# Performance work log

Measured on AMD Instinct MI355X. Metric: run time of the kernel, lower is better.

Reference implementation:

```python
import jax, jax.numpy as jnp
import numpy as np

DEPTH, DIM, HEADS, MLP_HID, POS_DIM, PROJ_DIM, NCLS, INP = 5, 128, 8, 256, 128, 128, 1000, 35
EPS = 1e-5

def _ln(x, g, b):
    m = x.mean(-1, keepdims=True)
    v = ((x - m) ** 2).mean(-1, keepdims=True)
    return (x - m) / jnp.sqrt(v + EPS) * g + b

def _gelu(x):
    return jax.nn.gelu(x, approximate=False)  # torch nn.GELU default (erf)

def setup_inputs() -> dict:
    key = jax.random.key(0)
    ks = iter(jax.random.split(key, 80))
    nxt = lambda: next(ks)
    B, N = 8, 1024
    w = lambda *s: (jax.random.normal(nxt(), s, jnp.float32) / np.sqrt(s[-2]).astype(np.float32))
    z = lambda *s: jnp.zeros(s, jnp.float32)
    o = lambda *s: jnp.ones(s, jnp.float32)
    node_feat = jax.random.normal(nxt(), (B, N, 3), jnp.float32)
    a = (jax.random.uniform(nxt(), (B, N, N)) < 0.01).astype(jnp.float32)
    adj = jnp.maximum(a, a.transpose(0, 2, 1))  # symmetric 0/1 adjacency
    lapl = jax.random.normal(nxt(), (B, N, 32), jnp.float32) * 0.1
    d = dict(
        node_feat=node_feat, adj=adj, lapl=lapl,
        cls_token=jax.random.normal(nxt(), (1, 1, DIM), jnp.float32),
        pe_w1=w(INP, 2 * INP), pe_b1=z(2 * INP),
        pe_w2=w(2 * INP, 2 * INP), pe_b2=z(2 * INP),
        pe_w3=w(2 * INP, 2 * INP), pe_b3=z(2 * INP),
        pe_lng=o(2 * INP), pe_lnb=z(2 * INP),
        pe_w4=w(2 * INP, POS_DIM), pe_b4=z(POS_DIM),
        blk_ln1_g=o(DEPTH, DIM), blk_ln1_b=z(DEPTH, DIM),
        blk_qkv_w=w(DEPTH, DIM, 3 * HEADS * DIM),
        blk_proj_w=w(DEPTH, HEADS * DIM, DIM), blk_proj_b=z(DEPTH, DIM),
        blk_gamma_w=jax.random.uniform(nxt(), (DEPTH, DIM, 2), jnp.float32) * 0.01,
        blk_gamma_b=z(DEPTH, 2),
        blk_ln2_g=o(DEPTH, DIM), blk_ln2_b=z(DEPTH, DIM),
        blk_mlp_w1=w(DEPTH, DIM, MLP_HID), blk_mlp_b1=z(DEPTH, MLP_HID),
        blk_mlp_w2=w(DEPTH, MLP_HID, DIM), blk_mlp_b2=z(DEPTH, DIM),
        head_lng=o(DIM), head_lnb=z(DIM), head_w=w(DIM, DIM), head_b=z(DIM),
        proj_w1=w(DIM, PROJ_DIM), proj_b1=z(PROJ_DIM),
        proj_w2=w(PROJ_DIM, PROJ_DIM), proj_b2=z(PROJ_DIM),
        proj_w3=w(PROJ_DIM, PROJ_DIM), proj_b3=z(PROJ_DIM),
        proj_lng=o(PROJ_DIM), proj_lnb=z(PROJ_DIM),
        proj_w4=w(PROJ_DIM, NCLS), proj_b4=z(NCLS),
    )
    return d

def reference(node_feat, adj, lapl, cls_token, pe_w1, pe_b1, pe_w2, pe_b2, pe_w3, pe_b3,
              pe_lng, pe_lnb, pe_w4, pe_b4, blk_ln1_g, blk_ln1_b, blk_qkv_w, blk_proj_w,
              blk_proj_b, blk_gamma_w, blk_gamma_b, blk_ln2_g, blk_ln2_b, blk_mlp_w1,
              blk_mlp_b1, blk_mlp_w2, blk_mlp_b2, head_lng, head_lnb, head_w, head_b,
              proj_w1, proj_b1, proj_w2, proj_b2, proj_w3, proj_b3, proj_lng, proj_lnb,
              proj_w4, proj_b4):
    B, N, _ = node_feat.shape
    M = N + 1
    # positional-encoding MLP on concatenated [node_feat | lapl] (inp_dim = 35)
    x = jnp.concatenate([node_feat, lapl], axis=2)
    x = _gelu(x @ pe_w1 + pe_b1)
    x = _gelu(x @ pe_w2 + pe_b2)
    x = _gelu(x @ pe_w3 + pe_b3)
    x = _ln(x, pe_lng, pe_lnb) @ pe_w4 + pe_b4  # [B,N,DIM]
    x = jnp.concatenate([jnp.broadcast_to(cls_token, (B, 1, DIM)), x], axis=1)  # [B,M,DIM]
    # adjacency with cls row/col, adj_cls[:,0,0] = 1
    adj_cls = jnp.zeros((B, M, M), x.dtype).at[:, 0, 0].set(1.0).at[:, 1:, 1:].set(adj)
    scale = DIM ** (-0.5)
    for i in range(DEPTH):
        h = _ln(x, blk_ln1_g[i], blk_ln1_b[i])
        qkv = (h @ blk_qkv_w[i]).reshape(B, M, 3, HEADS, DIM).transpose(2, 0, 3, 1, 4)
        q, k, v = qkv[0], qkv[1], qkv[2]  # each [B,H,M,D]
        attn = jnp.einsum('bhnd,bhmd->bhnm', q, k) * scale
        gamma = jnp.exp(h @ blk_gamma_w[i] + blk_gamma_b[i])  # [B,M,2], use_exp=True
        attn = gamma[:, None, :, 0:1] * attn + gamma[:, None, :, 1:2] * adj_cls[:, None]
        attn = jax.nn.softmax(attn, axis=-1)
        o = jnp.einsum('bhnm,bhmd->bhnd', attn, v).transpose(0, 2, 1, 3).reshape(B, M, HEADS * DIM)
        x = o @ blk_proj_w[i] + blk_proj_b[i] + h  # residual from normed input (as in source)
        h2 = _ln(x, blk_ln2_g[i], blk_ln2_b[i])
        x = _gelu(h2 @ blk_mlp_w1[i] + blk_mlp_b1[i]) @ blk_mlp_w2[i] + blk_mlp_b2[i] + h2
    c = x[:, 0]
    c = _ln(c, head_lng, head_lnb) @ head_w + head_b  # mlp_head
    p = _gelu(c @ proj_w1 + proj_b1)
    p = _gelu(p @ proj_w2 + proj_b2)
    p = _gelu(p @ proj_w3 + proj_b3)
    p = _ln(p, proj_lng, proj_lnb) @ proj_w4 + proj_b4
    return (c, p)
```

## Files before the change

kernel.cpp:

```cpp
#include <hip/hip_runtime.h>
#include <hip/hip_bf16.h>
#include <math.h>

#define NB 8
#define NSEQ 1024
#define M_ 1025
#define ROWS (NB * M_)
#define DIMC 128
#define NHEADS 8
#define QKV3 3072
#define PEROWS (NB * NSEQ)
#define ACS 1088

typedef __attribute__((ext_vector_type(8))) short bf16x8;
typedef __attribute__((ext_vector_type(4))) float f32x4;

__device__ __forceinline__ float gelu_f(float x) {
  return 0.5f * x * (1.f + erff(x * 0.70710678118654752440f));
}

__device__ __forceinline__ unsigned short f2bf(float f) {
  __hip_bfloat16 h = __float2bfloat16(f);
  return *reinterpret_cast<unsigned short*>(&h);
}

__device__ __forceinline__ float bf2f(unsigned short u) {
  union { unsigned int i; float f; } c;
  c.i = ((unsigned int)u) << 16;
  return c.f;
}

__device__ __forceinline__ void g2lds16(const void* g, void* l) {
  __builtin_amdgcn_global_load_lds(
      (__attribute__((address_space(1))) void*)(g),
      (__attribute__((address_space(3))) void*)(l), 16, 0, 0);
}

template<int K, int KP, int C, int SS, int DOGELU>
__device__ __forceinline__ void pe_stage(
    int tid, const float* __restrict__ W, const float* __restrict__ B,
    const float* src, float* dst, float (*wb)[128])
{
  for (int i = tid; i < K * C; i += 128) wb[i / C][i % C] = W[i];
  if (tid < C) {
#pragma unroll
    for (int k = K; k < KP; ++k) wb[k][tid] = 0.f;
  }
  __syncthreads();
  if (tid < C) {
    float acc[16];
#pragma unroll
    for (int r = 0; r < 16; ++r) acc[r] = B[tid];
#pragma unroll 1
    for (int k4 = 0; k4 < KP; k4 += 4) {
      const float w0 = wb[k4 + 0][tid];
      const float w1 = wb[k4 + 1][tid];
      const float w2 = wb[k4 + 2][tid];
      const float w3 = wb[k4 + 3][tid];
#pragma unroll
      for (int r = 0; r < 16; ++r) {
        const float4 av = *(const float4*)&src[r * SS + k4];
        acc[r] = fmaf(av.x, w0, acc[r]);
        acc[r] = fmaf(av.y, w1, acc[r]);
        acc[r] = fmaf(av.z, w2, acc[r]);
        acc[r] = fmaf(av.w, w3, acc[r]);
      }
    }
#pragma unroll
    for (int r = 0; r < 16; ++r) dst[r * 72 + tid] = DOGELU ? gelu_f(acc[r]) : acc[r];
  }
  __syncthreads();
}

__global__ __launch_bounds__(128) void pe_fused_k(
    const float* __restrict__ nf, const float* __restrict__ lp,
    const float* __restrict__ w1, const float* __restrict__ b1,
    const float* __restrict__ w2, const float* __restrict__ b2,
    const float* __restrict__ w3, const float* __restrict__ b3,
    const float* __restrict__ lng, const float* __restrict__ lnb,
    const float* __restrict__ w4, const float* __restrict__ b4,
    float* __restrict__ x)
{
  __shared__ float sIn[16][36];
  __shared__ float sX[16][72];
  __shared__ float sY[16][72];
  __shared__ float wb[72][128];
  const int tid = threadIdx.x;
  const int r0 = blockIdx.x * 16;

  for (int i = tid; i < 16 * 35; i += 128) {
    const int r = i / 35, c = i - r * 35;
    const int gr = r0 + r;
    sIn[r][c] = (c < 3) ? nf[(size_t)gr * 3 + c] : lp[(size_t)gr * 32 + (c - 3)];
  }
  if (tid < 16) {
    sIn[tid][35] = 0.f;
    sX[tid][70] = 0.f; sX[tid][71] = 0.f;
    sY[tid][70] = 0.f; sY[tid][71] = 0.f;
  }
  __syncthreads();

  pe_stage<35, 36, 70, 36, 1>(tid, w1, b1, &sIn[0][0], &sX[0][0], wb);
  pe_stage<70, 72, 70, 72, 1>(tid, w2, b2, &sX[0][0], &sY[0][0], wb);
  pe_stage<70, 72, 70, 72, 1>(tid, w3, b3, &sY[0][0], &sX[0][0], wb);

  if (tid < 16) {
    float m = 0.f;
    for (int d = 0; d < 70; ++d) m += sX[tid][d];
    m *= (1.f / 70.f);
    float v = 0.f;
    for (int d = 0; d < 70; ++d) { const float t = sX[tid][d] - m; v += t * t; }
    const float inv = rsqrtf(v * (1.f / 70.f) + 1e-5f);
    for (int d = 0; d < 70; ++d) sX[tid][d] = (sX[tid][d] - m) * inv * lng[d] + lnb[d];
  }
  __syncthreads();

  {
    for (int i = tid; i < 70 * 128; i += 128) wb[i >> 7][i & 127] = w4[i];
#pragma unroll
    for (int k = 70; k < 72; ++k) wb[k][tid] = 0.f;
    __syncthreads();
    float acc[16];
#pragma unroll
    for (int r = 0; r < 16; ++r) acc[r] = b4[tid];
#pragma unroll 1
    for (int k4 = 0; k4 < 72; k4 += 4) {
      const float w0 = wb[k4 + 0][tid];
      const float w1v = wb[k4 + 1][tid];
      const float w2v = wb[k4 + 2][tid];
      const float w3v = wb[k4 + 3][tid];
#pragma unroll
      for (int r = 0; r < 16; ++r) {
        const float4 av = *(const float4*)&sX[r][k4];
        acc[r] = fmaf(av.x, w0, acc[r]);
        acc[r] = fmaf(av.y, w1v, acc[r]);
        acc[r] = fmaf(av.z, w2v, acc[r]);
        acc[r] = fmaf(av.w, w3v, acc[r]);
      }
    }
#pragma unroll
    for (int r = 0; r < 16; ++r) {
      const int gr = r0 + r;
      x[(size_t)(gr + gr / 1024 + 1) * DIMC + tid] = acc[r];
    }
  }
}

template<int ACT, int OBF, int RES>
__global__ __launch_bounds__(256) void mgemm_k(
    const unsigned short* __restrict__ Xb, const unsigned short* __restrict__ Wt,
    const float* __restrict__ bias, const float* __restrict__ res,
    void* __restrict__ outp, int rows, int K, int N)
{
  __shared__ unsigned short sX[64][72];
  __shared__ unsigned short sW[64][72];
  const int tid = threadIdx.x;
  const int w = tid >> 6, lane = tid & 63;
  const int col = lane & 15, quad = lane >> 4;
  const int r0 = blockIdx.x * 64, n0 = blockIdx.y * 64;
  const int lr = tid >> 2, lc = tid & 3;
  const int xrow = min(r0 + lr, rows - 1);
  const unsigned short* xsrc = Xb + (size_t)xrow * K + lc * 8;
  const unsigned short* wsrc = Wt + (size_t)(n0 + lr) * K + lc * 8;

  f32x4 acc[4];
#pragma unroll
  for (int t = 0; t < 4; ++t) acc[t] = (f32x4){0.f, 0.f, 0.f, 0.f};

  for (int k0 = 0; k0 < K; k0 += 64) {
    __syncthreads();
    *(uint4*)&sX[lr][lc * 8]      = *(const uint4*)(xsrc + k0);
    *(uint4*)&sX[lr][lc * 8 + 32] = *(const uint4*)(xsrc + k0 + 32);
    *(uint4*)&sW[lr][lc * 8]      = *(const uint4*)(wsrc + k0);
    *(uint4*)&sW[lr][lc * 8 + 32] = *(const uint4*)(wsrc + k0 + 32);
    __syncthreads();
    const bf16x8 aX0 = *(const bf16x8*)&sX[w * 16 + col][quad * 8];
    const bf16x8 aX1 = *(const bf16x8*)&sX[w * 16 + col][32 + quad * 8];
#pragma unroll
    for (int t = 0; t < 4; ++t) {
      const bf16x8 bW0 = *(const bf16x8*)&sW[t * 16 + col][quad * 8];
      const bf16x8 bW1 = *(const bf16x8*)&sW[t * 16 + col][32 + quad * 8];
      acc[t] = __builtin_amdgcn_mfma_f32_16x16x32_bf16(aX0, bW0, acc[t], 0, 0, 0);
      acc[t] = __builtin_amdgcn_mfma_f32_16x16x32_bf16(aX1, bW1, acc[t], 0, 0, 0);
    }
  }
  const int gr_base = r0 + w * 16 + quad * 4;
#pragma unroll
  for (int t = 0; t < 4; ++t) {
    const int n = n0 + t * 16 + col;
    const float bv = bias ? bias[n] : 0.f;
#pragma unroll
    for (int r = 0; r < 4; ++r) {
      const int gr = gr_base + r;
      if (gr < rows) {
        float v = acc[t][r] + bv;
        if (ACT) v = gelu_f(v);
        if (RES) v += res[(size_t)gr * N + n];
        if (OBF) ((unsigned short*)outp)[(size_t)gr * N + n] = f2bf(v);
        else     ((float*)outp)[(size_t)gr * N + n] = v;
      }
    }
  }
}

template<int DOLN, int GAMMA, int WRITEX>
__global__ __launch_bounds__(256) void mgemm_ln_k(
    const unsigned short* __restrict__ Xb, const unsigned short* __restrict__ Wt,
    const float* __restrict__ bias, const float* __restrict__ res,
    const float* __restrict__ lng, const float* __restrict__ lnb,
    const float* __restrict__ gw, const float* __restrict__ gb,
    float* __restrict__ xout, float* __restrict__ h,
    unsigned short* __restrict__ hb, float* __restrict__ gamout,
    int rows, int K)
{
  __shared__ unsigned short sX[32][72];
  __shared__ unsigned short sW[128][72];
  __shared__ float redS[2][32];
  __shared__ float redQ[2][32];
  __shared__ float redA0[2][32];
  __shared__ float redA1[2][32];
  const int tid = threadIdx.x;
  const int w = tid >> 6, lane = tid & 63;
  const int col = lane & 15, quad = lane >> 4;
  const int rg = w >> 1, ch = w & 1;
  const int r0 = blockIdx.x * 32;

  f32x4 acc[4];
#pragma unroll
  for (int t = 0; t < 4; ++t) acc[t] = (f32x4){0.f, 0.f, 0.f, 0.f};

  for (int k0 = 0; k0 < K; k0 += 64) {
    __syncthreads();
    {
      const int row = tid >> 3, c = tid & 7;
      const int xrow = min(r0 + row, rows - 1);
      *(uint4*)&sX[row][c * 8] = *(const uint4*)(Xb + (size_t)xrow * K + k0 + c * 8);
    }
#pragma unroll
    for (int l = 0; l < 4; ++l) {
      const int idx = l * 256 + tid;
      const int row = idx >> 3, c = idx & 7;
      *(uint4*)&sW[row][c * 8] = *(const uint4*)(Wt + (size_t)row * K + k0 + c * 8);
    }
    __syncthreads();
    const bf16x8 aX0 = *(const bf16x8*)&sX[rg * 16 + col][quad * 8];
    const bf16x8 aX1 = *(const bf16x8*)&sX[rg * 16 + col][32 + quad * 8];
#pragma unroll
    for (int t = 0; t < 4; ++t) {
      const bf16x8 bW0 = *(const bf16x8*)&sW[ch * 64 + t * 16 + col][quad * 8];
      const bf16x8 bW1 = *(const bf16x8*)&sW[ch * 64 + t * 16 + col][32 + quad * 8];
      acc[t] = __builtin_amdgcn_mfma_f32_16x16x32_bf16(aX0, bW0, acc[t], 0, 0, 0);
      acc[t] = __builtin_amdgcn_mfma_f32_16x16x32_bf16(aX1, bW1, acc[t], 0, 0, 0);
    }
  }

  const int gr_base = r0 + rg * 16 + quad * 4;
  float val[4][4];
#pragma unroll
  for (int r = 0; r < 4; ++r) {
    const int grc = min(gr_base + r, rows - 1);
#pragma unroll
    for (int t = 0; t < 4; ++t) {
      const int n = ch * 64 + t * 16 + col;
      val[t][r] = acc[t][r] + bias[n] + res[(size_t)grc * DIMC + n];
    }
  }
  if (WRITEX) {
#pragma unroll
    for (int r = 0; r < 4; ++r) {
      const int gr = gr_base + r;
      if (gr < rows) {
#pragma unroll
        for (int t = 0; t < 4; ++t)
          xout[(size_t)gr * DIMC + ch * 64 + t * 16 + col] = val[t][r];
      }
    }
  }
  if (DOLN) {
#pragma unroll
    for (int r = 0; r < 4; ++r) {
      float s = 0.f, q = 0.f;
#pragma unroll
      for (int t = 0; t < 4; ++t) { s += val[t][r]; q = fmaf(val[t][r], val[t][r], q); }
      s += __shfl_xor(s, 1); s += __shfl_xor(s, 2);
      s += __shfl_xor(s, 4); s += __shfl_xor(s, 8);
      q += __shfl_xor(q, 1); q += __shfl_xor(q, 2);
      q += __shfl_xor(q, 4); q += __shfl_xor(q, 8);
      if (col == 0) {
        const int rl = rg * 16 + quad * 4 + r;
        redS[ch][rl] = s;
        redQ[ch][rl] = q;
      }
    }
    __syncthreads();
    float lg[4], lb[4], gwa[4], gwb[4];
#pragma unroll
    for (int t = 0; t < 4; ++t) {
      const int n = ch * 64 + t * 16 + col;
      lg[t] = lng[n];
      lb[t] = lnb[n];
      if (GAMMA) { gwa[t] = gw[2 * n]; gwb[t] = gw[2 * n + 1]; }
    }
#pragma unroll
    for (int r = 0; r < 4; ++r) {
      const int rl = rg * 16 + quad * 4 + r;
      const int gr = gr_base + r;
      const float S = redS[0][rl] + redS[1][rl];
      const float Q = redQ[0][rl] + redQ[1][rl];
      const float mean = S * (1.f / 128.f);
      const float var = Q * (1.f / 128.f) - mean * mean;
      const float inv = rsqrtf(var + 1e-5f);
      float a0 = 0.f, a1 = 0.f;
#pragma unroll
      for (int t = 0; t < 4; ++t) {
        const float o = (val[t][r] - mean) * inv * lg[t] + lb[t];
        if (gr < rows) {
          const int n = ch * 64 + t * 16 + col;
          h[(size_t)gr * DIMC + n] = o;
          hb[(size_t)gr * DIMC + n] = f2bf(o);
        }
        if (GAMMA) { a0 = fmaf(o, gwa[t], a0); a1 = fmaf(o, gwb[t], a1); }
      }
      if (GAMMA) {
        a0 += __shfl_xor(a0, 1); a0 += __shfl_xor(a0, 2);
        a0 += __shfl_xor(a0, 4); a0 += __shfl_xor(a0, 8);
        a1 += __shfl_xor(a1, 1); a1 += __shfl_xor(a1, 2);
        a1 += __shfl_xor(a1, 4); a1 += __shfl_xor(a1, 8);
        if (col == 0) { redA0[ch][rl] = a0; redA1[ch][rl] = a1; }
      }
    }
    if (GAMMA) {
      __syncthreads();
#pragma unroll
      for (int r = 0; r < 4; ++r) {
        const int rl = rg * 16 + quad * 4 + r;
        const int gr = gr_base + r;
        if (ch == 0 && col == 0 && gr < rows) {
          gamout[(size_t)gr * 2 + 0] = expf(redA0[0][rl] + redA0[1][rl] + gb[0]);
          gamout[(size_t)gr * 2 + 1] = expf(redA1[0][rl] + redA1[1][rl] + gb[1]);
        }
      }
    }
  }
}

template<int OBF, int VT>
__global__ __launch_bounds__(256) void mgemm128_k(
    const unsigned short* __restrict__ Xb, const unsigned short* __restrict__ Wt,
    const float* __restrict__ bias, void* __restrict__ outp,
    unsigned short* __restrict__ vtp, int rows, int K, int N)
{
  __shared__ unsigned short sX[128][72];
  __shared__ unsigned short sW[128][72];
  const int tid = threadIdx.x;
  const int w = tid >> 6, lane = tid & 63;
  const int col = lane & 15, quad = lane >> 4;
  const int wr = w >> 1, wc = w & 1;
  const int r0 = blockIdx.x * 128, n0 = blockIdx.y * 128;

  f32x4 acc[4][4];
#pragma unroll
  for (int i = 0; i < 4; ++i)
#pragma unroll
    for (int j = 0; j < 4; ++j) acc[i][j] = (f32x4){0.f, 0.f, 0.f, 0.f};

  for (int k0 = 0; k0 < K; k0 += 64) {
    __syncthreads();
#pragma unroll
    for (int l = 0; l < 4; ++l) {
      const int idx = l * 256 + tid;
      const int row = idx >> 3, c = idx & 7;
      const int xrow = min(r0 + row, rows - 1);
      *(uint4*)&sX[row][c * 8] = *(const uint4*)(Xb + (size_t)xrow * K + k0 + c * 8);
      *(uint4*)&sW[row][c * 8] = *(const uint4*)(Wt + (size_t)(n0 + row) * K + k0 + c * 8);
    }
    __syncthreads();
    bf16x8 aX[4][2];
#pragma unroll
    for (int i = 0; i < 4; ++i) {
      aX[i][0] = *(const bf16x8*)&sX[wr * 64 + i * 16 + col][quad * 8];
      aX[i][1] = *(const bf16x8*)&sX[wr * 64 + i * 16 + col][32 + quad * 8];
    }
#pragma unroll
    for (int j = 0; j < 4; ++j) {
      const bf16x8 b0 = *(const bf16x8*)&sW[wc * 64 + j * 16 + col][quad * 8];
      const bf16x8 b1 = *(const bf16x8*)&sW[wc * 64 + j * 16 + col][32 + quad * 8];
#pragma unroll
      for (int i = 0; i < 4; ++i) {
        acc[i][j] = __builtin_amdgcn_mfma_f32_16x16x32_bf16(aX[i][0], b0, acc[i][j], 0, 0, 0);
        acc[i][j] = __builtin_amdgcn_mfma_f32_16x16x32_bf16(aX[i][1], b1, acc[i][j], 0, 0, 0);
      }
    }
  }
  const bool dovt = VT && (n0 >= 2048);
#pragma unroll
  for (int i = 0; i < 4; ++i) {
    const int gr_base = r0 + wr * 64 + i * 16 + quad * 4;
    int bb[4], mm[4];
    if (dovt) {
#pragma unroll
      for (int r = 0; r < 4; ++r) {
        const int gr = gr_base + r;
        bb[r] = gr / 1025;
        mm[r] = gr - bb[r] * 1025;
      }
    }
#pragma unroll
    for (int j = 0; j < 4; ++j) {
      const int n = n0 + wc * 64 + j * 16 + col;
      const float bv = bias ? bias[n] : 0.f;
      const int hh = (n - 2048) >> 7;
      const int d  = (n - 2048) & 127;
#pragma unroll
      for (int r = 0; r < 4; ++r) {
        const int gr = gr_base + r;
        if (gr < rows) {
          const float v = acc[i][j][r] + bv;
          const unsigned short bf = f2bf(v);
          if (OBF) ((unsigned short*)outp)[(size_t)gr * N + n] = bf;
          else     ((float*)outp)[(size_t)gr * N + n] = v;
          if (dovt) vtp[(((size_t)(bb[r] * NHEADS + hh) * DIMC + d) * ACS) + mm[r]] = bf;
        }
      }
    }
  }
}

__global__ __launch_bounds__(256) void ln_rows_k(
    const float* __restrict__ in, float* __restrict__ out,
    unsigned short* __restrict__ outb,
    const float* __restrict__ g, const float* __restrict__ b,
    const float* __restrict__ gw, const float* __restrict__ gb,
    float* __restrict__ gamout, int rows, int D)
{
  const int wv = (blockIdx.x * blockDim.x + threadIdx.x) >> 6;
  const int lane = threadIdx.x & 63;
  if (wv >= rows) return;
  const float* r = in + (size_t)wv * D;
  float s = 0.f;
  for (int d = lane; d < D; d += 64) s += r[d];
  for (int off = 32; off; off >>= 1) s += __shfl_down(s, off);
  const float mean = __shfl(s, 0) / (float)D;
  float v = 0.f;
  for (int d = lane; d < D; d += 64) { float t = r[d] - mean; v += t * t; }
  for (int off = 32; off; off >>= 1) v += __shfl_down(v, off);
  const float inv = rsqrtf(__shfl(v, 0) / (float)D + 1e-5f);
  float* orow = out + (size_t)wv * D;
  float a0 = 0.f, a1 = 0.f;
  for (int d = lane; d < D; d += 64) {
    const float o = (r[d] - mean) * inv * g[d] + b[d];
    orow[d] = o;
    if (outb) outb[(size_t)wv * D + d] = f2bf(o);
    if (gw) { a0 = fmaf(o, gw[2 * d], a0); a1 = fmaf(o, gw[2 * d + 1], a1); }
  }
  if (gw) {
    for (int off = 32; off; off >>= 1) { a0 += __shfl_down(a0, off); a1 += __shfl_down(a1, off); }
    if (lane == 0) {
      gamout[(size_t)wv * 2 + 0] = expf(a0 + gb[0]);
      gamout[(size_t)wv * 2 + 1] = expf(a1 + gb[1]);
    }
  }
}

__global__ __launch_bounds__(256) void adjp_k(const float* __restrict__ adj,
                                              unsigned long long* __restrict__ adjp)
{
  const int n = blockIdx.x;
  const int b = blockIdx.y;
  const int wv = threadIdx.x >> 6, lane = threadIdx.x & 63;
  for (int w = wv; w < 17; w += 4) {
    const int m = w * 64 + lane;
    float av = 0.f;
    if (n == 0) av = (m == 0) ? 1.f : 0.f;
    else if (m >= 1 && m <= NSEQ) av = adj[((size_t)b * NSEQ + (n - 1)) * NSEQ + (m - 1)];
    const unsigned long long mask = __ballot(av != 0.f);
    if (lane == 0) adjp[((size_t)b * M_ + n) * 17 + w] = mask;
  }
}

__global__ void wtrans_k(const float* __restrict__ W, unsigned short* __restrict__ Wt,
                         int K, int N)
{
  __shared__ float t[32][33];
  const int k0 = blockIdx.x * 32, n0 = blockIdx.y * 32;
  const float* Wd = W + (size_t)blockIdx.z * K * N;
  unsigned short* Wtd = Wt + (size_t)blockIdx.z * K * N;
  for (int i = threadIdx.y; i < 32; i += 8)
    t[i][threadIdx.x] = Wd[(size_t)(k0 + i) * N + n0 + threadIdx.x];
  __syncthreads();
  for (int i = threadIdx.y; i < 32; i += 8)
    Wtd[(size_t)(n0 + i) * K + k0 + threadIdx.x] = f2bf(t[threadIdx.x][i]);
}

__global__ __launch_bounds__(512) void attn_mfma_k(
    const unsigned short* __restrict__ qkv, const float* __restrict__ gamma,
    const unsigned long long* __restrict__ adjp, const unsigned short* __restrict__ vt,
    unsigned short* __restrict__ o)
{
  __shared__ unsigned short sK[2][64][128];
  __shared__ unsigned short sVt[2][128][64];
  __shared__ unsigned short sP[256][64];

  const int hh = blockIdx.x, qt = blockIdx.y, b = blockIdx.z;
  const int tid = threadIdx.x;
  const int w = tid >> 6;
  const int lane = tid & 63;
  const int col = lane & 15;
  const int quad = lane >> 4;
  const int qbase = qt * 256 + w * 32;
  const float scale = 0.088388347648318447f;

  bf16x8 aQ[2][4];
#pragma unroll
  for (int rg = 0; rg < 2; ++rg) {
    const int qrow = qbase + rg * 16 + col;
    const unsigned short* qp = qkv + ((size_t)(b * M_ + qrow)) * QKV3 + hh * DIMC + quad * 8;
#pragma unroll
    for (int c = 0; c < 4; ++c) aQ[rg][c] = *(const bf16x8*)(qp + c * 32);
  }
  float g0[2][4], g1[2][4];
  int adjo[2][4];
#pragma unroll
  for (int rg = 0; rg < 2; ++rg)
#pragma unroll
    for (int r = 0; r < 4; ++r) {
      const int nc = qbase + rg * 16 + quad * 4 + r;
      g0[rg][r] = gamma[(size_t)(b * M_ + nc) * 2 + 0] * scale;
      g1[rg][r] = gamma[(size_t)(b * M_ + nc) * 2 + 1];
      adjo[rg][r] = (b * M_ + nc) * 17;
    }

  float l_i[2][4] = {{0.f, 0.f, 0.f, 0.f}, {0.f, 0.f, 0.f, 0.f}};
  f32x4 Oacc[2][8];
#pragma unroll
  for (int rg = 0; rg < 2; ++rg)
#pragma unroll
    for (int t = 0; t < 8; ++t) Oacc[rg][t] = (f32x4){0.f, 0.f, 0.f, 0.f};

  const size_t vtbase = ((size_t)(b * NHEADS + hh)) * DIMC * ACS;

  auto stageK = [&](int buf, int kt_) {
#pragma unroll
    for (int l = 0; l < 2; ++l) {
      const int m = l * 32 + w * 4 + (lane >> 4);
      const int gm = min(kt_ * 64 + m, 1024);
      const unsigned short* src = qkv + ((size_t)(b * M_ + gm)) * QKV3 + 1024
                                  + hh * DIMC + (((lane & 15) ^ (m & 7)) * 8);
      g2lds16(src, &sK[buf][l * 32 + w * 4][0]);
    }
  };
  auto stageV = [&](int buf, int kt_) {
#pragma unroll
    for (int l = 0; l < 2; ++l) {
      const int d = l * 64 + w * 8 + (lane >> 3);
      const unsigned short* src = vt + vtbase + (size_t)d * ACS + kt_ * 64
                                  + (((lane & 7) ^ (d & 7)) * 8);
      g2lds16(src, &sVt[buf][l * 64 + w * 8][0]);
    }
  };

  stageK(0, 0);
  stageV(0, 0);

  int cur = 0;
  for (int kt = 0; kt < 17; ++kt) {
    const int m0 = kt * 64;
    asm volatile("s_waitcnt vmcnt(0)" ::: "memory");
    __builtin_amdgcn_s_barrier();
    __builtin_amdgcn_sched_barrier(0);

    const bool more = (kt < 16);
    if (more) {
      stageK(cur ^ 1, kt + 1);
      stageV(cur ^ 1, kt + 1);
    }

    unsigned long long mk[2][4];
#pragma unroll
    for (int rg = 0; rg < 2; ++rg)
#pragma unroll
      for (int r = 0; r < 4; ++r) mk[rg][r] = adjp[adjo[rg][r] + kt];

    f32x4 Sacc[2][4];
#pragma unroll
    for (int rg = 0; rg < 2; ++rg)
#pragma unroll
      for (int t = 0; t < 4; ++t) Sacc[rg][t] = (f32x4){0.f, 0.f, 0.f, 0.f};
    __builtin_amdgcn_s_setprio(1);
#pragma unroll
    for (int t = 0; t < 4; ++t) {
#pragma unroll
      for (int c = 0; c < 4; ++c) {
        const bf16x8 bK = *(const bf16x8*)&sK[cur][t * 16 + col][((c * 4 + quad) ^ (col & 7)) * 8];
        Sacc[0][t] = __builtin_amdgcn_mfma_f32_16x16x32_bf16(aQ[0][c], bK, Sacc[0][t], 0, 0, 0);
        Sacc[1][t] = __builtin_amdgcn_mfma_f32_16x16x32_bf16(aQ[1][c], bK, Sacc[1][t], 0, 0, 0);
      }
    }
    __builtin_amdgcn_s_setprio(0);

#pragma unroll
    for (int t = 0; t < 4; ++t) {
      const int m = m0 + t * 16 + col;
      const bool mv = (m < M_);
      const int chb = t * 2 + (col >> 3);
      const int sh = t * 16 + col;
#pragma unroll
      for (int rg = 0; rg < 2; ++rg)
#pragma unroll
        for (int r = 0; r < 4; ++r) {
          const float bias = ((mk[rg][r] >> sh) & 1ull) ? g1[rg][r] : 0.f;
          const float s = fmaf(g0[rg][r], Sacc[rg][t][r], bias);
          const float pv = mv ? __expf(s) : 0.f;
          l_i[rg][r] += pv;
          const int ql = w * 32 + rg * 16 + quad * 4 + r;
          sP[ql][((chb ^ (ql & 7)) * 8) + (col & 7)] = f2bf(pv);
        }
    }

    __builtin_amdgcn_s_setprio(1);
#pragma unroll
    for (int ch = 0; ch < 2; ++ch) {
      const int pr = w * 32 + col;
      const bf16x8 aP0 = *(const bf16x8*)&sP[pr][((ch * 4 + quad) ^ (col & 7)) * 8];
      const bf16x8 aP1 = *(const bf16x8*)&sP[pr + 16][((ch * 4 + quad) ^ (col & 7)) * 8];
#pragma unroll
      for (int t = 0; t < 8; ++t) {
        const bf16x8 bV = *(const bf16x8*)&sVt[cur][t * 16 + col][((ch * 4 + quad) ^ (col & 7)) * 8];
        Oacc[0][t] = __builtin_amdgcn_mfma_f32_16x16x32_bf16(aP0, bV, Oacc[0][t], 0, 0, 0);
        Oacc[1][t] = __builtin_amdgcn_mfma_f32_16x16x32_bf16(aP1, bV, Oacc[1][t], 0, 0, 0);
      }
    }
    __builtin_amdgcn_s_setprio(0);
    cur ^= 1;
  }

#pragma unroll
  for (int rg = 0; rg < 2; ++rg)
#pragma unroll
    for (int r = 0; r < 4; ++r) {
      float s = l_i[rg][r];
      s += __shfl_xor(s, 1);
      s += __shfl_xor(s, 2);
      s += __shfl_xor(s, 4);
      s += __shfl_xor(s, 8);
      const int n = qbase + rg * 16 + quad * 4 + r;
      const float invl = 1.f / s;
      unsigned short* orow = o + ((size_t)(b * M_ + n)) * (NHEADS * DIMC) + hh * DIMC + col;
#pragma unroll
      for (int t = 0; t < 8; ++t) orow[t * 16] = f2bf(Oacc[rg][t][r] * invl);
    }
}

__global__ __launch_bounds__(256) void cls_attn_k(
    const unsigned short* __restrict__ qkv, const float* __restrict__ gamma,
    const unsigned long long* __restrict__ adjp, const unsigned short* __restrict__ vt,
    unsigned short* __restrict__ o)
{
  __shared__ float qf[DIMC];
  __shared__ float pbuf[1056];
  __shared__ float lred[4];
  __shared__ float oshare[DIMC];
  const int hh = blockIdx.x & 7, b = blockIdx.x >> 3;
  const int tid = threadIdx.x;
  const size_t rowbase = (size_t)b * M_ + 1024;

  if (tid < DIMC) qf[tid] = bf2f(qkv[rowbase * QKV3 + hh * DIMC + tid]);
  __syncthreads();
  const float g0 = gamma[rowbase * 2 + 0] * 0.088388347648318447f;
  const float g1 = gamma[rowbase * 2 + 1];

  float lpart = 0.f;
  for (int m = tid; m < M_; m += 256) {
    const unsigned short* kp = qkv + ((size_t)(b * M_ + m)) * QKV3 + 1024 + hh * DIMC;
    float s = 0.f;
#pragma unroll
    for (int d0 = 0; d0 < DIMC; d0 += 8) {
      const bf16x8 kv = *(const bf16x8*)(kp + d0);
#pragma unroll
      for (int j = 0; j < 8; ++j)
        s = fmaf(bf2f((unsigned short)kv[j]), qf[d0 + j], s);
    }
    const unsigned long long mkv = adjp[rowbase * 17 + (m >> 6)];
    const float bias = ((mkv >> (m & 63)) & 1ull) ? g1 : 0.f;
    const float p = __expf(fmaf(g0, s, bias));
    pbuf[m] = p;
    lpart += p;
  }
  for (int off = 32; off; off >>= 1) lpart += __shfl_down(lpart, off);
  if ((tid & 63) == 0) lred[tid >> 6] = lpart;
  __syncthreads();
  const float linv = 1.f / (lred[0] + lred[1] + lred[2] + lred[3]);

  const int d = tid & 127, half = tid >> 7;
  const unsigned short* vrow = vt + ((size_t)(b * NHEADS + hh)) * DIMC * ACS + (size_t)d * ACS;
  float acc = 0.f;
  const int mstart = half * 512;
  const int mend = half ? 1024 : 512;
  for (int m0 = mstart; m0 < mend; m0 += 8) {
    const bf16x8 vv = *(const bf16x8*)(vrow + m0);
#pragma unroll
    for (int j = 0; j < 8; ++j)
      acc = fmaf(bf2f((unsigned short)vv[j]), pbuf[m0 + j], acc);
  }
  if (half) acc = fmaf(bf2f(vrow[1024]), pbuf[1024], acc);
  if (half == 0) oshare[d] = acc;
  __syncthreads();
  if (half == 1) {
    const float val = (oshare[d] + acc) * linv;
    o[rowbase * (NHEADS * DIMC) + hh * DIMC + d] = f2bf(val);
  }
}

template<int DOLN, int ACT>
__global__ __launch_bounds__(256) void hstage_k(
    const float* __restrict__ in, int in_stride,
    const float* __restrict__ lng, const float* __restrict__ lnb,
    const float* __restrict__ W, const float* __restrict__ bias,
    float* __restrict__ out)
{
  __shared__ float xn[8][128];
  __shared__ float red[128];
  const int tid = threadIdx.x;
  for (int i = tid; i < 1024; i += 256) {
    const int r = i >> 7, d = i & 127;
    xn[r][d] = in[(size_t)r * in_stride + d];
  }
  __syncthreads();
  if (DOLN) {
    const int wv = tid >> 6, lane = tid & 63;
    const int row = wv * 2 + (lane >> 5);
    const int l32 = lane & 31;
    float s = 0.f;
    for (int d = l32; d < 128; d += 32) s += xn[row][d];
    for (int off = 16; off; off >>= 1) s += __shfl_xor(s, off);
    const float mean = s * (1.f / 128.f);
    float v = 0.f;
    for (int d = l32; d < 128; d += 32) { const float t = xn[row][d] - mean; v += t * t; }
    for (int off = 16; off; off >>= 1) v += __shfl_xor(v, off);
    const float inv = rsqrtf(v * (1.f / 128.f) + 1e-5f);
    for (int d = l32; d < 128; d += 32)
      xn[row][d] = (xn[row][d] - mean) * inv * lng[d] + lnb[d];
    __syncthreads();
  }
  const int col = blockIdx.x * 16 + (tid & 15);
  const int row = (tid >> 4) & 7;
  const int ks = tid >> 7;
  float acc = 0.f;
  const int kb = ks * 64;
  for (int k = kb; k < kb + 64; ++k)
    acc = fmaf(xn[row][k], W[k * 128 + col], acc);
  if (ks) red[tid - 128] = acc;
  __syncthreads();
  if (!ks) {
    float v = acc + red[tid] + bias[col];
    if (ACT) v = gelu_f(v);
    out[row * 128 + col] = v;
  }
}

__global__ __launch_bounds__(256) void hfinal_k(
    const float* __restrict__ in,
    const float* __restrict__ plg, const float* __restrict__ plb,
    const float* __restrict__ W, const float* __restrict__ bias,
    float* __restrict__ out_p)
{
  __shared__ float xn[128];
  const int r = blockIdx.x & 7, cc = blockIdx.x >> 3;
  const int tid = threadIdx.x;
  const int lane = tid & 63;
  const float a = in[r * 128 + lane];
  const float b = in[r * 128 + 64 + lane];
  float s = a + b;
  for (int off = 32; off; off >>= 1) s += __shfl_xor(s, off);
  const float mean = s * (1.f / 128.f);
  const float t0 = a - mean, t1 = b - mean;
  float v = t0 * t0 + t1 * t1;
  for (int off = 32; off; off >>= 1) v += __shfl_xor(v, off);
  const float inv = rsqrtf(v * (1.f / 128.f) + 1e-5f);
  if (tid < 128) xn[tid] = (in[r * 128 + tid] - mean) * inv * plg[tid] + plb[tid];
  __syncthreads();
  const int col = cc * 250 + tid;
  if (tid < 250) {
    float acc = bias[col];
    for (int k = 0; k < 128; ++k)
      acc = fmaf(xn[k], W[(size_t)k * 1000 + col], acc);
    out_p[r * 1000 + col] = acc;
  }
}

__global__ void fill_cls_k(const float* __restrict__ cls, float* __restrict__ x)
{
  x[(size_t)blockIdx.x * M_ * DIMC + threadIdx.x] = cls[threadIdx.x];
}

extern "C" void kernel_launch(void* const* d_in, const int* in_sizes, int n_in,
                              void* d_out, int out_size, void* d_ws, size_t ws_size,
                              hipStream_t stream)
{
  (void)in_sizes; (void)n_in; (void)out_size; (void)ws_size;
  const float* node_feat = (const float*)d_in[0];
  const float* adj       = (const float*)d_in[1];
  const float* lapl      = (const float*)d_in[2];
  const float* cls_token = (const float*)d_in[3];
  const float* pe_w1 = (const float*)d_in[4];
  const float* pe_b1 = (const float*)d_in[5];
  const float* pe_w2 = (const float*)d_in[6];
  const float* pe_b2 = (const float*)d_in[7];
  const float* pe_w3 = (const float*)d_in[8];
  const float* pe_b3 = (const float*)d_in[9];
  const float* pe_lng = (const float*)d_in[10];
  const float* pe_lnb = (const float*)d_in[11];
  const float* pe_w4 = (const float*)d_in[12];
  const float* pe_b4 = (const float*)d_in[13];
  const float* blk_ln1_g = (const float*)d_in[14];
  const float* blk_ln1_b = (const float*)d_in[15];
  const float* blk_qkv_w = (const float*)d_in[16];
  const float* blk_proj_w = (const float*)d_in[17];
  const float* blk_proj_b = (const float*)d_in[18];
  const float* blk_gamma_w = (const float*)d_in[19];
  const float* blk_gamma_b = (const float*)d_in[20];
  const float* blk_ln2_g = (const float*)d_in[21];
  const float* blk_ln2_b = (const float*)d_in[22];
  const float* blk_mlp_w1 = (const float*)d_in[23];
  const float* blk_mlp_b1 = (const float*)d_in[24];
  const float* blk_mlp_w2 = (const float*)d_in[25];
  const float* blk_mlp_b2 = (const float*)d_in[26];
  const float* head_lng = (const float*)d_in[27];
  const float* head_lnb = (const float*)d_in[28];
  const float* head_w = (const float*)d_in[29];
  const float* head_b = (const float*)d_in[30];
  const float* proj_w1 = (const float*)d_in[31];
  const float* proj_b1 = (const float*)d_in[32];
  const float* proj_w2 = (const float*)d_in[33];
  const float* proj_b2 = (const float*)d_in[34];
  const float* proj_w3 = (const float*)d_in[35];
  const float* proj_b3 = (const float*)d_in[36];
  const float* proj_lng = (const float*)d_in[37];
  const float* proj_lnb = (const float*)d_in[38];
  const float* proj_w4 = (const float*)d_in[39];
  const float* proj_b4 = (const float*)d_in[40];

  float* ws   = (float*)d_ws;
  float* x    = ws;
  float* h    = x + 1049600;
  float* gam  = h + 1049600;
  float* obuf = gam + 16400;
  unsigned short* obufb = (unsigned short*)obuf;
  unsigned short* hidb  = (unsigned short*)(obuf + 4198400);
  float* sm  = obuf + 5248000;
  unsigned short* hb   = (unsigned short*)(sm + 8192);
  unsigned short* qkv  = hb + 1049600;
  unsigned long long* adjp = (unsigned long long*)(qkv + 25190400);
  unsigned short* vt   = (unsigned short*)(adjp + 139400 + 88);
  unsigned short* qkvWt = vt + 8912896;
  unsigned short* projWt = qkvWt + 5 * 393216;
  unsigned short* mlp1Wt = projWt + 5 * 131072;
  unsigned short* mlp2Wt = mlp1Wt + 5 * 32768;

  float* out_c = (float*)d_out;
  float* out_p = out_c + NB * DIMC;
  float* p1 = sm;
  float* p2 = sm + 1024;

  adjp_k<<<dim3(M_, NB), 256, 0, stream>>>(adj, adjp);
  wtrans_k<<<dim3(4, 96, 5), dim3(32, 8), 0, stream>>>(blk_qkv_w, qkvWt, 128, 3072);
  wtrans_k<<<dim3(32, 4, 5), dim3(32, 8), 0, stream>>>(blk_proj_w, projWt, 1024, 128);
  wtrans_k<<<dim3(4, 8, 5), dim3(32, 8), 0, stream>>>(blk_mlp_w1, mlp1Wt, 128, 256);
  wtrans_k<<<dim3(8, 4, 5), dim3(32, 8), 0, stream>>>(blk_mlp_w2, mlp2Wt, 256, 128);

  pe_fused_k<<<512, 128, 0, stream>>>(node_feat, lapl, pe_w1, pe_b1, pe_w2, pe_b2,
                                      pe_w3, pe_b3, pe_lng, pe_lnb, pe_w4, pe_b4, x);
  fill_cls_k<<<NB, DIMC, 0, stream>>>(cls_token, x);

  const int lnGrid = (ROWS * 64 + 255) / 256;
  ln_rows_k<<<lnGrid, 256, 0, stream>>>(x, h, hb, blk_ln1_g, blk_ln1_b,
                                        blk_gamma_w, blk_gamma_b, gam, ROWS, DIMC);

  const int fGrid = (ROWS + 31) / 32;
  for (int i = 0; i < 5; ++i) {
    const float* pb   = blk_proj_b + i * DIMC;
    const float* ln2g = blk_ln2_g + i * DIMC;
    const float* ln2b = blk_ln2_b + i * DIMC;
    const float* mb1  = blk_mlp_b1 + i * 256;
    const float* mb2  = blk_mlp_b2 + i * DIMC;
    const unsigned short* qw = qkvWt + (size_t)i * 393216;
    const unsigned short* pw = projWt + (size_t)i * 131072;
    const unsigned short* m1w = mlp1Wt + (size_t)i * 32768;
    const unsigned short* m2w = mlp2Wt + (size_t)i * 32768;

    mgemm128_k<1, 1><<<dim3(65, 24), 256, 0, stream>>>(hb, qw, nullptr, qkv, vt, ROWS, 128, 3072);
    attn_mfma_k<<<dim3(NHEADS, 4, NB), 512, 0, stream>>>(qkv, gam, adjp, vt, obufb);
    cls_attn_k<<<64, 256, 0, stream>>>(qkv, gam, adjp, vt, obufb);

    mgemm_ln_k<1, 0, 0><<<fGrid, 256, 0, stream>>>(
        obufb, pw, pb, h, ln2g, ln2b, nullptr, nullptr,
        nullptr, h, hb, nullptr, ROWS, 1024);

    mgemm_k<1, 1, 0><<<dim3(129, 4), 256, 0, stream>>>(hb, m1w, mb1, nullptr, hidb, ROWS, 128, 256);

    if (i < 4) {
      const float* nln1g = blk_ln1_g + (i + 1) * DIMC;
      const float* nln1b = blk_ln1_b + (i + 1) * DIMC;
      const float* ngw   = blk_gamma_w + (size_t)(i + 1) * DIMC * 2;
      const float* ngb   = blk_gamma_b + (i + 1) * 2;
      mgemm_ln_k<1, 1, 0><<<fGrid, 256, 0, stream>>>(
          hidb, m2w, mb2, h, nln1g, nln1b, ngw, ngb,
          nullptr, h, hb, gam, ROWS, 256);
    } else {
      mgemm_ln_k<0, 0, 1><<<fGrid, 256, 0, stream>>>(
          hidb, m2w, mb2, h, nullptr, nullptr, nullptr, nullptr,
          x, nullptr, nullptr, nullptr, ROWS, 256);
    }
  }

  hstage_k<1, 0><<<8, 256, 0, stream>>>(x, M_ * DIMC, head_lng, head_lnb,
                                        head_w, head_b, out_c);
  hstage_k<0, 1><<<8, 256, 0, stream>>>(out_c, 128, nullptr, nullptr,
                                        proj_w1, proj_b1, p1);
  hstage_k<0, 1><<<8, 256, 0, stream>>>(p1, 128, nullptr, nullptr,
                                        proj_w2, proj_b2, p2);
  hstage_k<0, 1><<<8, 256, 0, stream>>>(p2, 128, nullptr, nullptr,
                                        proj_w3, proj_b3, p1);
  hfinal_k<<<32, 256, 0, stream>>>(p1, proj_lng, proj_lnb, proj_w4, proj_b4, out_p);
}
```

Measured before the change: 1.326 ms.

## Fuse MLP up and down GEMMs with the hidden activation kept in LDS

The separate GEMM+GELU kernel and the second MLP GEMM+LayerNorm kernel become one kernel. Each 32-row block computes the 256-wide GELU hidden layer into shared memory, then loads W2 and does the down-projection, residual, next LayerNorm and gamma epilogue. This removes one launch per layer and the global write and read of the bf16 hidden tensor. In exchange each block reloads both full weight matrices and uses a large LDS footprint, which lowers occupancy. Separately, the QKV GEMM now skips the row-major V store when it already writes the transposed V copy.

```diff
diff --git a/kernel.cpp b/kernel.cpp
--- a/kernel.cpp
+++ b/kernel.cpp
@@ -146,58 +146,183 @@
   }
 }
 
-template<int ACT, int OBF, int RES>
-__global__ __launch_bounds__(256) void mgemm_k(
-    const unsigned short* __restrict__ Xb, const unsigned short* __restrict__ Wt,
-    const float* __restrict__ bias, const float* __restrict__ res,
-    void* __restrict__ outp, int rows, int K, int N)
-{
-  __shared__ unsigned short sX[64][72];
-  __shared__ unsigned short sW[64][72];
+template<int DOLN, int GAMMA, int WRITEX>
+__global__ __launch_bounds__(256) void mlp_fused_k(
+    const unsigned short* __restrict__ Xb, const unsigned short* __restrict__ W1t,
+    const float* __restrict__ b1, const unsigned short* __restrict__ W2t,
+    const float* __restrict__ b2, const float* __restrict__ res,
+    const float* __restrict__ lng, const float* __restrict__ lnb,
+    const float* __restrict__ gw, const float* __restrict__ gb,
+    float* __restrict__ xout, float* __restrict__ h,
+    unsigned short* __restrict__ hb, float* __restrict__ gamout, int rows)
+{
+  __shared__ unsigned short sX[32][136];
+  __shared__ unsigned short sW[256][136];
+  __shared__ unsigned short sHid[32][264];
+  __shared__ float redS[2][32];
+  __shared__ float redQ[2][32];
+  __shared__ float redA0[2][32];
+  __shared__ float redA1[2][32];
   const int tid = threadIdx.x;
   const int w = tid >> 6, lane = tid & 63;
   const int col = lane & 15, quad = lane >> 4;
-  const int r0 = blockIdx.x * 64, n0 = blockIdx.y * 64;
-  const int lr = tid >> 2, lc = tid & 3;
-  const int xrow = min(r0 + lr, rows - 1);
-  const unsigned short* xsrc = Xb + (size_t)xrow * K + lc * 8;
-  const unsigned short* wsrc = Wt + (size_t)(n0 + lr) * K + lc * 8;
+  const int rg = w >> 1, ch = w & 1;
+  const int r0 = blockIdx.x * 32;
+
+#pragma unroll
+  for (int l = 0; l < 2; ++l) {
+    const int idx = l * 256 + tid;
+    const int row = idx >> 4, c = idx & 15;
+    const int xrow = min(r0 + row, rows - 1);
+    *(uint4*)&sX[row][c * 8] = *(const uint4*)(Xb + (size_t)xrow * 128 + c * 8);
+  }
+#pragma unroll
+  for (int l = 0; l < 16; ++l) {
+    const int idx = l * 256 + tid;
+    const int row = idx >> 4, c = idx & 15;
+    *(uint4*)&sW[row][c * 8] = *(const uint4*)(W1t + (size_t)row * 128 + c * 8);
+  }
+  __syncthreads();
+
+  {
+    bf16x8 aX[4];
+#pragma unroll
+    for (int kc = 0; kc < 4; ++kc)
+      aX[kc] = *(const bf16x8*)&sX[rg * 16 + col][kc * 32 + quad * 8];
+    f32x4 accA[8];
+#pragma unroll
+    for (int t = 0; t < 8; ++t) accA[t] = (f32x4){0.f, 0.f, 0.f, 0.f};
+#pragma unroll
+    for (int t = 0; t < 8; ++t) {
+#pragma unroll
+      for (int kc = 0; kc < 4; ++kc) {
+        const bf16x8 bW = *(const bf16x8*)&sW[ch * 128 + t * 16 + col][kc * 32 + quad * 8];
+        accA[t] = __builtin_amdgcn_mfma_f32_16x16x32_bf16(aX[kc], bW, accA[t], 0, 0, 0);
+      }
+    }
+#pragma unroll
+    for (int t = 0; t < 8; ++t) {
+      const int n = ch * 128 + t * 16 + col;
+      const float bv = b1[n];
+#pragma unroll
+      for (int r = 0; r < 4; ++r)
+        sHid[rg * 16 + quad * 4 + r][n] = f2bf(gelu_f(accA[t][r] + bv));
+    }
+  }
+  __syncthreads();
+
+  unsigned short (*sW2)[264] = (unsigned short(*)[264])&sW[0][0];
+#pragma unroll
+  for (int l = 0; l < 16; ++l) {
+    const int idx = l * 256 + tid;
+    const int row = idx >> 5, c = idx & 31;
+    *(uint4*)&sW2[row][c * 8] = *(const uint4*)(W2t + (size_t)row * 256 + c * 8);
+  }
+  __syncthreads();
 
   f32x4 acc[4];
 #pragma unroll
   for (int t = 0; t < 4; ++t) acc[t] = (f32x4){0.f, 0.f, 0.f, 0.f};
-
-  for (int k0 = 0; k0 < K; k0 += 64) {
-    __syncthreads();
-    *(uint4*)&sX[lr][lc * 8]      = *(const uint4*)(xsrc + k0);
-    *(uint4*)&sX[lr][lc * 8 + 32] = *(const uint4*)(xsrc + k0 + 32);
-    *(uint4*)&sW[lr][lc * 8]      = *(const uint4*)(wsrc + k0);
-    *(uint4*)&sW[lr][lc * 8 + 32] = *(const uint4*)(wsrc + k0 + 32);
-    __syncthreads();
-    const bf16x8 aX0 = *(const bf16x8*)&sX[w * 16 + col][quad * 8];
-    const bf16x8 aX1 = *(const bf16x8*)&sX[w * 16 + col][32 + quad * 8];
+  {
+    bf16x8 aH[8];
+#pragma unroll
+    for (int ks = 0; ks < 8; ++ks)
+      aH[ks] = *(const bf16x8*)&sHid[rg * 16 + col][ks * 32 + quad * 8];
 #pragma unroll
     for (int t = 0; t < 4; ++t) {
-      const bf16x8 bW0 = *(const bf16x8*)&sW[t * 16 + col][quad * 8];
-      const bf16x8 bW1 = *(const bf16x8*)&sW[t * 16 + col][32 + quad * 8];
-      acc[t] = __builtin_amdgcn_mfma_f32_16x16x32_bf16(aX0, bW0, acc[t], 0, 0, 0);
-      acc[t] = __builtin_amdgcn_mfma_f32_16x16x32_bf16(aX1, bW1, acc[t], 0, 0, 0);
-    }
-  }
-  const int gr_base = r0 + w * 16 + quad * 4;
-#pragma unroll
-  for (int t = 0; t < 4; ++t) {
-    const int n = n0 + t * 16 + col;
-    const float bv = bias ? bias[n] : 0.f;
+#pragma unroll
+      for (int ks = 0; ks < 8; ++ks) {
+        const bf16x8 bW = *(const bf16x8*)&sW2[ch * 64 + t * 16 + col][ks * 32 + quad * 8];
+        acc[t] = __builtin_amdgcn_mfma_f32_16x16x32_bf16(aH[ks], bW, acc[t], 0, 0, 0);
+      }
+    }
+  }
+
+  const int gr_base = r0 + rg * 16 + quad * 4;
+  float val[4][4];
+#pragma unroll
+  for (int r = 0; r < 4; ++r) {
+    const int grc = min(gr_base + r, rows - 1);
+#pragma unroll
+    for (int t = 0; t < 4; ++t) {
+      const int n = ch * 64 + t * 16 + col;
+      val[t][r] = acc[t][r] + b2[n] + res[(size_t)grc * DIMC + n];
+    }
+  }
+  if (WRITEX) {
 #pragma unroll
     for (int r = 0; r < 4; ++r) {
       const int gr = gr_base + r;
       if (gr < rows) {
-        float v = acc[t][r] + bv;
-        if (ACT) v = gelu_f(v);
-        if (RES) v += res[(size_t)gr * N + n];
-        if (OBF) ((unsigned short*)outp)[(size_t)gr * N + n] = f2bf(v);
-        else     ((float*)outp)[(size_t)gr * N + n] = v;
+#pragma unroll
+        for (int t = 0; t < 4; ++t)
+          xout[(size_t)gr * DIMC + ch * 64 + t * 16 + col] = val[t][r];
+      }
+    }
+  }
+  if (DOLN) {
+#pragma unroll
+    for (int r = 0; r < 4; ++r) {
+      float s = 0.f, q = 0.f;
+#pragma unroll
+      for (int t = 0; t < 4; ++t) { s += val[t][r]; q = fmaf(val[t][r], val[t][r], q); }
+      s += __shfl_xor(s, 1); s += __shfl_xor(s, 2);
+      s += __shfl_xor(s, 4); s += __shfl_xor(s, 8);
+      q += __shfl_xor(q, 1); q += __shfl_xor(q, 2);
+      q += __shfl_xor(q, 4); q += __shfl_xor(q, 8);
+      if (col == 0) {
+        const int rl = rg * 16 + quad * 4 + r;
+        redS[ch][rl] = s;
+        redQ[ch][rl] = q;
+      }
+    }
+    __syncthreads();
+    float lg[4], lb[4], gwa[4], gwb[4];
+#pragma unroll
+    for (int t = 0; t < 4; ++t) {
+      const int n = ch * 64 + t * 16 + col;
+      lg[t] = lng[n];
+      lb[t] = lnb[n];
+      if (GAMMA) { gwa[t] = gw[2 * n]; gwb[t] = gw[2 * n + 1]; }
+    }
+#pragma unroll
+    for (int r = 0; r < 4; ++r) {
+      const int rl = rg * 16 + quad * 4 + r;
+      const int gr = gr_base + r;
+      const float S = redS[0][rl] + redS[1][rl];
+      const float Q = redQ[0][rl] + redQ[1][rl];
+      const float mean = S * (1.f / 128.f);
+      const float var = Q * (1.f / 128.f) - mean * mean;
+      const float inv = rsqrtf(var + 1e-5f);
+      float a0 = 0.f, a1 = 0.f;
+#pragma unroll
+      for (int t = 0; t < 4; ++t) {
+        const float o = (val[t][r] - mean) * inv * lg[t] + lb[t];
+        if (gr < rows) {
+          const int n = ch * 64 + t * 16 + col;
+          h[(size_t)gr * DIMC + n] = o;
+          hb[(size_t)gr * DIMC + n] = f2bf(o);
+        }
+        if (GAMMA) { a0 = fmaf(o, gwa[t], a0); a1 = fmaf(o, gwb[t], a1); }
+      }
+      if (GAMMA) {
+        a0 += __shfl_xor(a0, 1); a0 += __shfl_xor(a0, 2);
+        a0 += __shfl_xor(a0, 4); a0 += __shfl_xor(a0, 8);
+        a1 += __shfl_xor(a1, 1); a1 += __shfl_xor(a1, 2);
+        a1 += __shfl_xor(a1, 4); a1 += __shfl_xor(a1, 8);
+        if (col == 0) { redA0[ch][rl] = a0; redA1[ch][rl] = a1; }
+      }
+    }
+    if (GAMMA) {
+      __syncthreads();
+#pragma unroll
+      for (int r = 0; r < 4; ++r) {
+        const int rl = rg * 16 + quad * 4 + r;
+        const int gr = gr_base + r;
+        if (ch == 0 && col == 0 && gr < rows) {
+          gamout[(size_t)gr * 2 + 0] = expf(redA0[0][rl] + redA0[1][rl] + gb[0]);
+          gamout[(size_t)gr * 2 + 1] = expf(redA1[0][rl] + redA1[1][rl] + gb[1]);
+        }
       }
     }
   }
@@ -417,9 +542,12 @@
         if (gr < rows) {
           const float v = acc[i][j][r] + bv;
           const unsigned short bf = f2bf(v);
-          if (OBF) ((unsigned short*)outp)[(size_t)gr * N + n] = bf;
-          else     ((float*)outp)[(size_t)gr * N + n] = v;
-          if (dovt) vtp[(((size_t)(bb[r] * NHEADS + hh) * DIMC + d) * ACS) + mm[r]] = bf;
+          if (dovt) {
+            vtp[(((size_t)(bb[r] * NHEADS + hh) * DIMC + d) * ACS) + mm[r]] = bf;
+          } else {
+            if (OBF) ((unsigned short*)outp)[(size_t)gr * N + n] = bf;
+            else     ((float*)outp)[(size_t)gr * N + n] = v;
+          }
         }
       }
     }
@@ -856,6 +984,7 @@
   unsigned short* projWt = qkvWt + 5 * 393216;
   unsigned short* mlp1Wt = projWt + 5 * 131072;
   unsigned short* mlp2Wt = mlp1Wt + 5 * 32768;
+  (void)hidb;
 
   float* out_c = (float*)d_out;
   float* out_p = out_c + NB * DIMC;
@@ -896,20 +1025,18 @@
         obufb, pw, pb, h, ln2g, ln2b, nullptr, nullptr,
         nullptr, h, hb, nullptr, ROWS, 1024);
 
-    mgemm_k<1, 1, 0><<<dim3(129, 4), 256, 0, stream>>>(hb, m1w, mb1, nullptr, hidb, ROWS, 128, 256);
-
     if (i < 4) {
       const float* nln1g = blk_ln1_g + (i + 1) * DIMC;
       const float* nln1b = blk_ln1_b + (i + 1) * DIMC;
       const float* ngw   = blk_gamma_w + (size_t)(i + 1) * DIMC * 2;
       const float* ngb   = blk_gamma_b + (i + 1) * 2;
-      mgemm_ln_k<1, 1, 0><<<fGrid, 256, 0, stream>>>(
-          hidb, m2w, mb2, h, nln1g, nln1b, ngw, ngb,
-          nullptr, h, hb, gam, ROWS, 256);
+      mlp_fused_k<1, 1, 0><<<fGrid, 256, 0, stream>>>(
+          hb, m1w, mb1, m2w, mb2, h, nln1g, nln1b, ngw, ngb,
+          nullptr, h, hb, gam, ROWS);
     } else {
-      mgemm_ln_k<0, 0, 1><<<fGrid, 256, 0, stream>>>(
-          hidb, m2w, mb2, h, nullptr, nullptr, nullptr, nullptr,
-          x, nullptr, nullptr, nullptr, ROWS, 256);
+      mlp_fused_k<0, 0, 1><<<fGrid, 256, 0, stream>>>(
+          hb, m1w, mb1, m2w, mb2, h, nullptr, nullptr, nullptr, nullptr,
+          x, nullptr, nullptr, nullptr, ROWS);
     }
   }
 
```

Measured after the change: 1.328 ms. Within noise of the previous version (+0.1%).
